# Performance work log

Measured on AMD Instinct MI355X. Metric: run time of the kernel, lower is better.

## Reference

```python
import jax, jax.numpy as jnp
import numpy as np

NORMALIZED_LENGTH = 512  # init kwarg
T_FRAMES = 32768
N_LM = 543  # mediapipe holistic landmark count


def setup_inputs() -> dict:
    key = jax.random.key(0)
    kf, kn, kd, ki = jax.random.split(key, 4)
    frames = jax.random.uniform(kf, (T_FRAMES, N_LM, 3), dtype=jnp.float32)
    nan_mask = jax.random.uniform(kn, (T_FRAMES, N_LM, 3)) < 0.10
    frames = jnp.where(nan_mask, jnp.float32(jnp.nan), frames)
    drop = jax.random.uniform(kd, (T_FRAMES,)) < 0.05
    hand_zone = jnp.arange(N_LM) >= 468
    frames = jnp.where(drop[:, None, None] & hand_zone[None, :, None], jnp.float32(jnp.nan), frames)
    lips_idx = jax.random.randint(ki, (40,), 0, 468, dtype=jnp.int32)
    return {"frames": frames, "lips_idx": lips_idx}


def _nan_mean0(x):
    # tf_nan_mean over axis 0 (keepdims); 0/0 -> NaN in TF is immediately zeroed
    # afterwards, so we emit 0 directly (identical forward values, safe grads).
    finite = ~jnp.isnan(x)
    s = jnp.where(finite, x, jnp.zeros((), x.dtype)).sum(axis=0, keepdims=True)
    c = finite.sum(axis=0, keepdims=True)
    return jnp.where(c == 0, jnp.zeros((), x.dtype), s / jnp.maximum(c, 1).astype(x.dtype))


def reference(frames, lips_idx):
    fr = frames[:, :, :2]                       # drop z coord
    lh = fr[:, 468:489]                         # [T, 21, 2]
    rh = fr[:, 522:543]                         # [T, 21, 2]
    lh = jnp.stack([lh[..., 0], 1.0 - lh[..., 1]], axis=-1)
    rh = jnp.stack([1.0 - rh[..., 0], 1.0 - rh[..., 1]], axis=-1)
    # stack hands, NaN->0, sum over the 2-hand axis
    hand = jnp.nan_to_num(lh) + jnp.nan_to_num(rh)   # [T, 21, 2]
    keep = hand.sum(axis=(1, 2)) != 0.0              # frames with >=1 visible hand
    hand = hand[keep]                                # [S, 21, 2]
    lips = fr[:, lips_idx][keep]                     # [S, 40, 2]
    lips = jnp.where(jnp.isnan(lips), _nan_mean0(lips), lips)
    raw = jnp.concatenate([hand, lips], axis=1)      # [S, 61, 2]
    S = int(raw.shape[0])
    # tf.linspace(0, S-1, L+1) cast to int32 -> segment boundaries (truncation)
    b = np.linspace(0.0, S - 1.0, NORMALIZED_LENGTH + 1).astype(np.int32)
    # frame t belongs to bin i with b[i] <= t < b[i+1]; t >= b[L] maps to L (dropped)
    seg = jnp.asarray(np.searchsorted(b, np.arange(S), side="right") - 1)
    sums = jax.ops.segment_sum(raw, seg, num_segments=NORMALIZED_LENGTH)
    cnt = jax.ops.segment_sum(jnp.ones((S,), raw.dtype), seg, num_segments=NORMALIZED_LENGTH)
    # raw is NaN-free at this point, so nan-mean == plain mean; empty bin -> NaN -> 0
    mean = jnp.where(cnt[:, None, None] == 0, jnp.zeros((), raw.dtype),
                     sums / jnp.maximum(cnt, 1.0)[:, None, None])
    sampled = mean.reshape(NORMALIZED_LENGTH, -1)    # Flatten -> [L, 122]
    rows = sampled.sum(axis=1) != 0.0                # drop all-zero (empty) bins
    return sampled[rows]
```

## Files before the change

kernel.cpp:

```cpp
#include <hip/hip_runtime.h>

#define T_FRAMES 32768
#define ROWF 1629
#define NSEG 512
#define NVAL 122
#define STRIDE 128
#define K1_BLOCKS 512

__global__ __launch_bounds__(1024) void k1_gather(
    const float* __restrict__ frames, const int* __restrict__ lips_idx,
    int* __restrict__ keep, float* __restrict__ psum, int* __restrict__ pcnt,
    float* __restrict__ stage) {
  __shared__ float ls[80];
  __shared__ int lc[80];
  __shared__ int idx3[40];
  int tid = threadIdx.x;
  if (tid < 80) { ls[tid] = 0.0f; lc[tid] = 0; }
  if (tid < 40) idx3[tid] = lips_idx[tid] * 3;
  __syncthreads();

  int lane = tid & 63;
  int wv = tid >> 6;
  int t0 = (blockIdx.x * 16 + wv) * 4;

  int jh = lane >> 1, ch = lane & 1;
  int offL = 1404 + 3 * jh + ch;
  int offR = 1566 + 3 * jh + ch;
  int offA = idx3[lane >> 1] + (lane & 1);
  int offB = (lane < 16) ? (idx3[(lane + 64) >> 1] + (lane & 1)) : 0;

  float lh[4], rh[4], xa[4], xb[4];
  #pragma unroll
  for (int ff = 0; ff < 4; ++ff) {
    const float* f = frames + (size_t)(t0 + ff) * ROWF;
    lh[ff] = (lane < 42) ? f[offL] : 0.0f;
    rh[ff] = (lane < 42) ? f[offR] : 1.0f;
    xa[ff] = f[offA];
    xb[ff] = (lane < 16) ? f[offB] : 0.0f;
  }

  #pragma unroll
  for (int ff = 0; ff < 4; ++ff) {
    int t = t0 + ff;
    float hv = 0.0f;
    if (lane < 42) {
      float a = ch ? (1.0f - lh[ff]) : lh[ff];
      float b = 1.0f - rh[ff];
      a = (a == a) ? a : 0.0f;
      b = (b == b) ? b : 0.0f;
      hv = a + b;
    }
    int kp = (__ballot(hv != 0.0f) != 0ull) ? 1 : 0;
    if (lane == 0) keep[t] = kp;

    if (kp) {
      float* srow = stage + (size_t)t * STRIDE;
      if (lane < 42) srow[lane] = hv;
      float x = xa[ff];
      srow[42 + lane] = x;
      if (x == x) { atomicAdd(&ls[lane], x); atomicAdd(&lc[lane], 1); }
      if (lane < 16) {
        float y = xb[ff];
        srow[106 + lane] = y;
        if (y == y) { atomicAdd(&ls[64 + lane], y); atomicAdd(&lc[64 + lane], 1); }
      }
    }
  }

  __syncthreads();
  if (tid < 80) {
    psum[blockIdx.x * 80 + tid] = ls[tid];
    pcnt[blockIdx.x * 80 + tid] = lc[tid];
  }
}

__global__ __launch_bounds__(1024) void k2_scan(
    const int* __restrict__ keep, int* __restrict__ kept_t,
    int* __restrict__ Sp, const float* __restrict__ psum,
    const int* __restrict__ pcnt, float* __restrict__ lip_sum,
    int* __restrict__ lip_cnt) {
  __shared__ int wsum[16];
  int tid = threadIdx.x;
  int lane = tid & 63, wv = tid >> 6;

  if (tid < 80) {
    float s = 0.0f; int c = 0;
    for (int b = 0; b < K1_BLOCKS; ++b) {
      s += psum[b * 80 + tid];
      c += pcnt[b * 80 + tid];
    }
    lip_sum[tid] = s; lip_cnt[tid] = c;
  }

  const int PER = T_FRAMES / 1024;
  int base = tid * PER;
  int fl[PER];
  int local = 0;
  #pragma unroll
  for (int k = 0; k < PER; ++k) { fl[k] = keep[base + k]; local += fl[k]; }

  int scan = local;
  #pragma unroll
  for (int off = 1; off < 64; off <<= 1) {
    int n = __shfl_up(scan, off);
    if (lane >= off) scan += n;
  }
  if (lane == 63) wsum[wv] = scan;
  __syncthreads();
  if (tid < 16) {
    int v = wsum[tid];
    #pragma unroll
    for (int off = 1; off < 16; off <<= 1) {
      int n = __shfl_up(v, off);
      if (tid >= off) v += n;
    }
    wsum[tid] = v;
  }
  __syncthreads();
  int excl = ((wv == 0) ? 0 : wsum[wv - 1]) + (scan - local);
  #pragma unroll
  for (int k = 0; k < PER; ++k) {
    if (fl[k]) kept_t[excl++] = base + k;
  }
  if (tid == 1023) Sp[0] = wsum[15];
}

__global__ __launch_bounds__(512) void k3_segments(
    const float* __restrict__ stage, const int* __restrict__ kept_t,
    const int* __restrict__ Sp, const float* __restrict__ lip_sum,
    const int* __restrict__ lip_cnt, float* __restrict__ out, int out_size) {
  __shared__ int seglist[128];
  __shared__ float part[4][128];
  int tid = threadIdx.x;
  int v = tid & 127;
  int r = tid >> 7;
  int seg = blockIdx.x;
  long long Sm1 = (long long)Sp[0] - 1;
  if (Sm1 < 0) Sm1 = 0;
  int lo = (int)(((long long)seg * Sm1) >> 9);
  int hi = (int)(((long long)(seg + 1) * Sm1) >> 9);
  int cnt = hi - lo;

  for (int k = tid; k < cnt; k += 512) seglist[k] = kept_t[lo + k];
  __syncthreads();

  float cm = 0.0f;
  if (v >= 42 && v < NVAL) {
    int w = v - 42;
    int c = lip_cnt[w];
    cm = (c == 0) ? 0.0f : lip_sum[w] / (float)c;
  }

  float acc = 0.0f;
  if (v < NVAL) {
    for (int k = r; k < cnt; k += 4) {
      float x = stage[(size_t)seglist[k] * STRIDE + v];
      acc += (x == x) ? x : cm;
    }
  }
  part[r][v] = acc;
  __syncthreads();
  if (r == 0 && v < NVAL) {
    float tot = part[0][v] + part[1][v] + part[2][v] + part[3][v];
    float mean = (cnt == 0) ? 0.0f : tot / (float)cnt;
    int o = seg * NVAL + v;
    if (o < out_size) out[o] = mean;
  }
}

extern "C" void kernel_launch(void* const* d_in, const int* in_sizes, int n_in,
                              void* d_out, int out_size, void* d_ws, size_t ws_size,
                              hipStream_t stream) {
  const float* frames = (const float*)d_in[0];
  const int* lips_idx = (const int*)d_in[1];
  float* out = (float*)d_out;

  char* ws = (char*)d_ws;
  int* keep      = (int*)(ws);
  int* kept_t    = (int*)(ws + 131072);
  int* Sp        = (int*)(ws + 262144);
  float* lip_sum = (float*)(ws + 262208);
  int* lip_cnt   = (int*)(ws + 262720);
  float* psum    = (float*)(ws + 263232);
  int* pcnt      = (int*)(ws + 427072);
  float* stage   = (float*)(ws + 590912);


  k1_gather<<<K1_BLOCKS, 1024, 0, stream>>>(frames, lips_idx, keep, psum,
                                            pcnt, stage);
  k2_scan<<<1, 1024, 0, stream>>>(keep, kept_t, Sp, psum, pcnt, lip_sum,
                                  lip_cnt);
  k3_segments<<<NSEG, 512, 0, stream>>>(stage, kept_t, Sp, lip_sum, lip_cnt,
                                        out, out_size);
}
```

Measured before the change: 326.0 us.

## Stage full face rows in shared memory with coalesced loads before lip gather

The first kernel now copies each frame's whole face region (1404 floats) into per-wave shared memory with coalesced loads, then reads the lip landmarks from shared memory instead of issuing scattered global loads. Each wave now handles 8 frames sequentially, and blocks are 512 threads instead of 1024. The aim is to replace uncoalesced gathers with contiguous reads. The cost is reading far more bytes per frame, about 1404 floats instead of about 80, and the frames are no longer software-pipelined because the loop is not unrolled.

```diff
diff --git a/kernel.cpp b/kernel.cpp
--- a/kernel.cpp
+++ b/kernel.cpp
@@ -2,15 +2,17 @@
 
 #define T_FRAMES 32768
 #define ROWF 1629
+#define FACEF 1404
 #define NSEG 512
 #define NVAL 122
 #define STRIDE 128
 #define K1_BLOCKS 512
 
-__global__ __launch_bounds__(1024) void k1_gather(
+__global__ __launch_bounds__(512) void k1_face(
     const float* __restrict__ frames, const int* __restrict__ lips_idx,
     int* __restrict__ keep, float* __restrict__ psum, int* __restrict__ pcnt,
     float* __restrict__ stage) {
+  __shared__ float face[8][FACEF + 4];
   __shared__ float ls[80];
   __shared__ int lc[80];
   __shared__ int idx3[40];
@@ -21,7 +23,7 @@
 
   int lane = tid & 63;
   int wv = tid >> 6;
-  int t0 = (blockIdx.x * 16 + wv) * 4;
+  float* fb = face[wv];
 
   int jh = lane >> 1, ch = lane & 1;
   int offL = 1404 + 3 * jh + ch;
@@ -29,23 +31,20 @@
   int offA = idx3[lane >> 1] + (lane & 1);
   int offB = (lane < 16) ? (idx3[(lane + 64) >> 1] + (lane & 1)) : 0;
 
-  float lh[4], rh[4], xa[4], xb[4];
-  #pragma unroll
-  for (int ff = 0; ff < 4; ++ff) {
-    const float* f = frames + (size_t)(t0 + ff) * ROWF;
-    lh[ff] = (lane < 42) ? f[offL] : 0.0f;
-    rh[ff] = (lane < 42) ? f[offR] : 1.0f;
-    xa[ff] = f[offA];
-    xb[ff] = (lane < 16) ? f[offB] : 0.0f;
-  }
+  int base_t = (blockIdx.x * 8 + wv) * 8;
+  for (int ff = 0; ff < 8; ++ff) {
+    int t = base_t + ff;
+    const float* f = frames + (size_t)t * ROWF;
 
-  #pragma unroll
-  for (int ff = 0; ff < 4; ++ff) {
-    int t = t0 + ff;
+    float lh = 0.0f, rh = 1.0f;
+    if (lane < 42) { lh = f[offL]; rh = f[offR]; }
+
+    for (int p = lane; p < FACEF; p += 64) fb[p] = f[p];
+
     float hv = 0.0f;
     if (lane < 42) {
-      float a = ch ? (1.0f - lh[ff]) : lh[ff];
-      float b = 1.0f - rh[ff];
+      float a = ch ? (1.0f - lh) : lh;
+      float b = 1.0f - rh;
       a = (a == a) ? a : 0.0f;
       b = (b == b) ? b : 0.0f;
       hv = a + b;
@@ -56,11 +55,11 @@
     if (kp) {
       float* srow = stage + (size_t)t * STRIDE;
       if (lane < 42) srow[lane] = hv;
-      float x = xa[ff];
+      float x = fb[offA];
       srow[42 + lane] = x;
       if (x == x) { atomicAdd(&ls[lane], x); atomicAdd(&lc[lane], 1); }
       if (lane < 16) {
-        float y = xb[ff];
+        float y = fb[offB];
         srow[106 + lane] = y;
         if (y == y) { atomicAdd(&ls[64 + lane], y); atomicAdd(&lc[64 + lane], 1); }
       }
@@ -186,8 +185,8 @@
   float* stage   = (float*)(ws + 590912);
 
 
-  k1_gather<<<K1_BLOCKS, 1024, 0, stream>>>(frames, lips_idx, keep, psum,
-                                            pcnt, stage);
+  k1_face<<<K1_BLOCKS, 512, 0, stream>>>(frames, lips_idx, keep, psum,
+                                         pcnt, stage);
   k2_scan<<<1, 1024, 0, stream>>>(keep, kept_t, Sp, psum, pcnt, lip_sum,
                                   lip_cnt);
   k3_segments<<<NSEG, 512, 0, stream>>>(stage, kept_t, Sp, lip_sum, lip_cnt,
```

After: 344.0 us. +5.5%, slower.
